# Performance work log

Measured on AMD Instinct MI355X. Metric: run time of the kernel, lower is better.

The kernel has to match this reference:

```python
import jax, jax.numpy as jnp
import numpy as np

NUM_HEADS = 16
EPS = 1e-5  # torch nn.LayerNorm default


def _ln(x, g, b):
    m = jnp.mean(x, axis=-1, keepdims=True)
    v = jnp.var(x, axis=-1, keepdims=True)
    return (x - m) / jnp.sqrt(v + EPS) * g + b


def _attn(q, k, v, proj_w, proj_b):
    B, N, C = q.shape
    S = k.shape[1]
    H = NUM_HEADS
    D = C // H
    qh = q.reshape(B, N, H, D).transpose(0, 2, 1, 3)
    kh = k.reshape(B, S, H, D).transpose(0, 2, 1, 3)
    vh = v.reshape(B, S, H, D).transpose(0, 2, 1, 3)
    scores = jnp.einsum('bhnd,bhsd->bhns', qh, kh) * (D ** -0.5)
    aw = jax.nn.softmax(scores, axis=-1)
    o = jnp.einsum('bhns,bhsd->bhnd', aw, vh)
    o = o.transpose(0, 2, 1, 3).reshape(B, N, C)
    return o @ proj_w + proj_b


def _mlp(x, w1, b1, w2, b2):
    h = jax.nn.gelu(x @ w1 + b1, approximate=False)  # torch nn.GELU (exact erf)
    return h @ w2 + b2


def setup_inputs() -> dict:
    key = jax.random.key(0)
    ks = jax.random.split(key, 12)
    B, N, C = 4, 512, 1024
    H = 4 * C
    s = 0.02
    return {
        'x': jax.random.normal(ks[0], (B, N, C), jnp.float32),
        'y': jax.random.normal(ks[1], (B, N, C), jnp.float32),
        'norm1_g': jnp.ones((C,), jnp.float32),
        'norm1_b': jnp.zeros((C,), jnp.float32),
        'norm2_g': jnp.ones((C,), jnp.float32),
        'norm2_b': jnp.zeros((C,), jnp.float32),
        'proj_w': jax.random.normal(ks[2], (C, C), jnp.float32) * s,
        'proj_b': jnp.zeros((C,), jnp.float32),
        'fc1_w': jax.random.normal(ks[3], (C, H), jnp.float32) * s,
        'fc1_b': jnp.zeros((H,), jnp.float32),
        'fc2_w': jax.random.normal(ks[4], (H, C), jnp.float32) * s,
        'fc2_b': jnp.zeros((C,), jnp.float32),
        'is_selfatt': 1,
    }


def reference(x, y, norm1_g, norm1_b, norm2_g, norm2_b, proj_w, proj_b,
              fc1_w, fc1_b, fc2_w, fc2_b, is_selfatt):
    for _ in range(4):
        if is_selfatt:
            xn = _ln(x, norm1_g, norm1_b)
            x = x + _attn(xn, xn, xn, proj_w, proj_b)
            x = x + _mlp(_ln(x, norm2_g, norm2_b), fc1_w, fc1_b, fc2_w, fc2_b)
            yn = _ln(y, norm1_g, norm1_b)
            y = y + _attn(yn, yn, yn, proj_w, proj_b)
            y = y + _mlp(_ln(y, norm2_g, norm2_b), fc1_w, fc1_b, fc2_w, fc2_b)
        xn = _ln(x, norm1_g, norm1_b)
        yn = _ln(y, norm1_g, norm1_b)
        x1 = x + _attn(xn, yn, yn, proj_w, proj_b)
        x1 = x1 + _mlp(_ln(x1, norm2_g, norm2_b), fc1_w, fc1_b, fc2_w, fc2_b)
        y1 = y + _attn(yn, xn, xn, proj_w, proj_b)
        y1 = y1 + _mlp(_ln(y1, norm2_g, norm2_b), fc1_w, fc1_b, fc2_w, fc2_b)
    return (x1, y1)
```

## Files before the change

### kernel.cpp

```cpp
#include <hip/hip_runtime.h>
#include <hip/hip_bf16.h>
#include <math.h>

#define BDIM 4
#define SEQ 512
#define CH 1024
#define NH 16
#define HD 64
#define HIDN 4096
#define ROWS (BDIM * SEQ)
#define MROWS (2 * ROWS)
#define BHTOT (BDIM * NH)

using bf16 = __hip_bfloat16;
typedef __attribute__((ext_vector_type(4))) float f32x4;
typedef __attribute__((ext_vector_type(8))) short bf16x8;

typedef __attribute__((address_space(1))) const unsigned int GU32;
typedef __attribute__((address_space(3))) unsigned int LU32;

__device__ __forceinline__ void gload16(const bf16* g, bf16* l) {
  __builtin_amdgcn_global_load_lds((GU32*)g, (LU32*)l, 16, 0, 0);
}

__global__ __launch_bounds__(256) void ln_bf16_kernel(
    const float* __restrict__ x, const float* __restrict__ g,
    const float* __restrict__ b, bf16* __restrict__ out) {
  int row = blockIdx.x;
  int t = threadIdx.x;
  const float4 v = reinterpret_cast<const float4*>(x + (size_t)row * CH)[t];
  float s = v.x + v.y + v.z + v.w;
  float s2 = v.x * v.x + v.y * v.y + v.z * v.z + v.w * v.w;
#pragma unroll
  for (int o = 32; o > 0; o >>= 1) {
    s += __shfl_down(s, o);
    s2 += __shfl_down(s2, o);
  }
  __shared__ float red[10];
  int lane = t & 63, wid = t >> 6;
  if (lane == 0) { red[wid] = s; red[4 + wid] = s2; }
  __syncthreads();
  if (t == 0) {
    float ts = red[0] + red[1] + red[2] + red[3];
    float ts2 = red[4] + red[5] + red[6] + red[7];
    float mean = ts * (1.0f / CH);
    float var = ts2 * (1.0f / CH) - mean * mean;
    red[8] = mean;
    red[9] = rsqrtf(var + 1e-5f);
  }
  __syncthreads();
  float mean = red[8], rstd = red[9];
  const float4 gv = reinterpret_cast<const float4*>(g)[t];
  const float4 bv = reinterpret_cast<const float4*>(b)[t];
  alignas(8) bf16 o4[4];
  o4[0] = __float2bfloat16((v.x - mean) * rstd * gv.x + bv.x);
  o4[1] = __float2bfloat16((v.y - mean) * rstd * gv.y + bv.y);
  o4[2] = __float2bfloat16((v.z - mean) * rstd * gv.z + bv.z);
  o4[3] = __float2bfloat16((v.w - mean) * rstd * gv.w + bv.w);
  reinterpret_cast<uint2*>(out + (size_t)row * CH)[t] = *reinterpret_cast<const uint2*>(o4);
}

__global__ __launch_bounds__(256) void head_transpose_kernel(
    const bf16* __restrict__ src, bf16* __restrict__ dst) {
  __shared__ bf16 t[32][33];
  int bh = blockIdx.z, b = bh >> 4, h = bh & 15;
  int s0 = blockIdx.x * 32, d0 = blockIdx.y * 32;
  int tx = threadIdx.x & 31, ty = threadIdx.x >> 5;
  const bf16* sp = src + ((size_t)(b * SEQ + s0)) * CH + h * HD + d0;
  for (int i = ty; i < 32; i += 8) t[i][tx] = sp[(size_t)i * CH + tx];
  __syncthreads();
  bf16* dp = dst + ((size_t)bh * HD + d0) * SEQ + s0;
  for (int i = ty; i < 32; i += 8) dp[(size_t)i * SEQ + tx] = t[tx][i];
}

__global__ __launch_bounds__(256) void wt_transpose_kernel(
    const float* __restrict__ W, bf16* __restrict__ WT, int K, int Nout) {
  __shared__ float t[32][33];
  int k0 = blockIdx.x * 32, n0 = blockIdx.y * 32;
  int tx = threadIdx.x & 31, ty = threadIdx.x >> 5;
  for (int i = ty; i < 32; i += 8)
    t[i][tx] = W[(size_t)(k0 + i) * Nout + n0 + tx];
  __syncthreads();
  for (int i = ty; i < 32; i += 8)
    WT[(size_t)(n0 + i) * K + k0 + tx] = __float2bfloat16(t[tx][i]);
}

template <int MODE, int RING>
__global__ __launch_bounds__(256) void gemm128(
    const bf16* __restrict__ A, int lda,
    const bf16* __restrict__ Bt, int ldb,
    void* __restrict__ Cout, int ldc,
    const float* __restrict__ base, const float* __restrict__ bias,
    int K) {
  int m0 = blockIdx.x * 128, n0 = blockIdx.y * 128;
  __shared__ bf16 As[RING][128 * 32];
  __shared__ bf16 Bs[RING][128 * 32];
  int tid = threadIdx.x, wid = tid >> 6, lane = tid & 63;
  int wr = wid >> 1, wc = wid & 1;
  int srow = tid >> 2;
  int scol = ((tid & 3) ^ (srow & 3)) << 3;
  const bf16* ga = &A[(size_t)(m0 + srow) * lda + scol];
  const bf16* gb = &Bt[(size_t)(n0 + srow) * ldb + scol];
  int fr = lane & 15, kr = lane >> 4;
  f32x4 acc[4][4] = {};

  auto stage = [&](int b, int k0) {
    gload16(ga + k0, As[b] + tid * 8);
    gload16(ga + (size_t)64 * lda + k0, As[b] + 2048 + tid * 8);
    gload16(gb + k0, Bs[b] + tid * 8);
    gload16(gb + (size_t)64 * ldb + k0, Bs[b] + 2048 + tid * 8);
  };
  auto compute = [&](int b) {
    bf16x8 aF[4], bF[4];
#pragma unroll
    for (int m = 0; m < 4; ++m) {
      int R = wr * 64 + m * 16 + fr;
      aF[m] = *reinterpret_cast<const bf16x8*>(&As[b][R * 32 + ((kr ^ (R & 3)) << 3)]);
    }
#pragma unroll
    for (int n = 0; n < 4; ++n) {
      int R = wc * 64 + n * 16 + fr;
      bF[n] = *reinterpret_cast<const bf16x8*>(&Bs[b][R * 32 + ((kr ^ (R & 3)) << 3)]);
    }
#pragma unroll
    for (int m = 0; m < 4; ++m)
#pragma unroll
      for (int n = 0; n < 4; ++n)
        acc[m][n] = __builtin_amdgcn_mfma_f32_16x16x32_bf16(aF[m], bF[n], acc[m][n], 0, 0, 0);
  };

  int nt = K / 32;
#pragma unroll
  for (int i = 0; i < RING - 1; ++i) stage(i, i * 32);
  for (int t = 0; t < nt; ++t) {
    int rem = nt - 1 - t;
    if (rem >= RING - 1) {
      stage((t + RING - 1) % RING, (t + RING - 1) * 32);
      if (RING == 4) asm volatile("s_waitcnt vmcnt(12)" ::: "memory");
      else           asm volatile("s_waitcnt vmcnt(8)" ::: "memory");
    } else if (rem == 2) {
      asm volatile("s_waitcnt vmcnt(8)" ::: "memory");
    } else if (rem == 1) {
      asm volatile("s_waitcnt vmcnt(4)" ::: "memory");
    } else {
      asm volatile("s_waitcnt vmcnt(0)" ::: "memory");
    }
    __builtin_amdgcn_s_barrier();
    __builtin_amdgcn_sched_barrier(0);
    compute(t % RING);
    __builtin_amdgcn_s_barrier();
  }

  int colL = lane & 15;
  int rbase = (lane >> 4) * 4;
#pragma unroll
  for (int n = 0; n < 4; ++n) {
    int gc = n0 + wc * 64 + n * 16 + colL;
    float bv = bias ? bias[gc] : 0.0f;
#pragma unroll
    for (int m = 0; m < 4; ++m)
#pragma unroll
      for (int j = 0; j < 4; ++j) {
        int gr = m0 + wr * 64 + m * 16 + rbase + j;
        float v = acc[m][n][j] + bv;
        size_t idx = (size_t)gr * ldc + gc;
        if (MODE == 0) {
          ((float*)Cout)[idx] = base[idx] + v;
        } else {
          float gl = 0.5f * v * (1.0f + erff(v * 0.70710678118654752f));
          ((bf16*)Cout)[idx] = __float2bfloat16(gl);
        }
      }
  }
}

__global__ __launch_bounds__(512) void attn_fused(
    const bf16* __restrict__ ln1, const bf16* __restrict__ vT,
    bf16* __restrict__ out, int xorb) {
  __shared__ bf16 kv[3][64 * 64];
  __shared__ bf16 Pl[128 * 512];
  int bh = blockIdx.y;
  int b = bh >> 4, h = bh & 15;
  int kvb = b ^ xorb;
  int kvbh = kvb * NH + h;
  int m0 = blockIdx.x * 128;
  int tid = threadIdx.x, wid = tid >> 6, lane = tid & 63;
  int fr = lane & 15, kr = lane >> 4;
  int srow = tid >> 3;
  int scol8 = ((tid & 7) ^ (srow & 7)) << 3;
  const bf16* kbase = ln1 + ((size_t)(kvb * SEQ + srow)) * CH + h * HD + scol8;
  const bf16* vbase = vT + ((size_t)kvbh * HD + srow) * SEQ + scol8;

  int qrow = m0 + wid * 16 + fr;
  const bf16* qbase = ln1 + ((size_t)(b * SEQ) + qrow) * CH + h * HD;
  bf16x8 qF0 = *reinterpret_cast<const bf16x8*>(qbase + kr * 8);
  bf16x8 qF1 = *reinterpret_cast<const bf16x8*>(qbase + 32 + kr * 8);

  f32x4 acc[32];
#pragma unroll
  for (int n = 0; n < 32; ++n) acc[n] = (f32x4){0.f, 0.f, 0.f, 0.f};

  gload16(kbase, kv[0] + tid * 8);
  gload16(kbase + (size_t)64 * CH, kv[1] + tid * 8);
#pragma unroll
  for (int c = 0; c < 8; ++c) {
    if (c + 2 < 8) gload16(kbase + (size_t)(c + 2) * 64 * CH, kv[(c + 2) % 3] + tid * 8);
    if (c + 2 < 8)      asm volatile("s_waitcnt vmcnt(2)" ::: "memory");
    else if (c + 1 < 8) asm volatile("s_waitcnt vmcnt(1)" ::: "memory");
    else                asm volatile("s_waitcnt vmcnt(0)" ::: "memory");
    __builtin_amdgcn_s_barrier();
    __builtin_amdgcn_sched_barrier(0);
    const char* kb = (const char*)kv[c % 3];
#pragma unroll
    for (int nf = 0; nf < 4; ++nf) {
      int sl = nf * 16 + fr;
      int byt = sl * 128 + kr * 16;
      bf16x8 k0 = *reinterpret_cast<const bf16x8*>(kb + (byt ^ ((sl & 7) << 4)));
      bf16x8 k1 = *reinterpret_cast<const bf16x8*>(kb + ((byt + 64) ^ ((sl & 7) << 4)));
      acc[c * 4 + nf] = __builtin_amdgcn_mfma_f32_16x16x32_bf16(qF0, k0, acc[c * 4 + nf], 0, 0, 0);
      acc[c * 4 + nf] = __builtin_amdgcn_mfma_f32_16x16x32_bf16(qF1, k1, acc[c * 4 + nf], 0, 0, 0);
    }
    __builtin_amdgcn_s_barrier();
  }

  float mx[4], sum[4], inv[4];
#pragma unroll
  for (int j = 0; j < 4; ++j) {
    float m = acc[0][j];
#pragma unroll
    for (int n = 1; n < 32; ++n) m = fmaxf(m, acc[n][j]);
    m = fmaxf(m, __shfl_xor(m, 1));
    m = fmaxf(m, __shfl_xor(m, 2));
    m = fmaxf(m, __shfl_xor(m, 4));
    m = fmaxf(m, __shfl_xor(m, 8));
    mx[j] = m * 0.125f;
  }
#pragma unroll
  for (int j = 0; j < 4; ++j) sum[j] = 0.f;
#pragma unroll
  for (int n = 0; n < 32; ++n)
#pragma unroll
    for (int j = 0; j < 4; ++j) {
      float p = exp2f((acc[n][j] * 0.125f - mx[j]) * 1.4426950408889634f);
      acc[n][j] = p;
      sum[j] += p;
    }
#pragma unroll
  for (int j = 0; j < 4; ++j) {
    float s = sum[j];
    s += __shfl_xor(s, 1);
    s += __shfl_xor(s, 2);
    s += __shfl_xor(s, 4);
    s += __shfl_xor(s, 8);
    inv[j] = 1.0f / s;
  }
  {
    char* pb = (char*)Pl;
#pragma unroll
    for (int n = 0; n < 32; ++n)
#pragma unroll
      for (int j = 0; j < 4; ++j) {
        int pr = wid * 16 + (lane >> 4) * 4 + j;
        int pc = fr + 16 * n;
        int byt = (pr * 1024 + pc * 2) ^ ((pr & 7) << 4);
        *reinterpret_cast<bf16*>(pb + byt) = __float2bfloat16(acc[n][j]);
      }
  }

  f32x4 oacc[4] = {};
  int prow = wid * 16 + fr;
  gload16(vbase, kv[0] + tid * 8);
  gload16(vbase + 64, kv[1] + tid * 8);
#pragma unroll
  for (int c = 0; c < 8; ++c) {
    if (c + 2 < 8) gload16(vbase + (size_t)(c + 2) * 64, kv[(c + 2) % 3] + tid * 8);
    if (c + 2 < 8)      asm volatile("s_waitcnt vmcnt(2)" ::: "memory");
    else if (c + 1 < 8) asm volatile("s_waitcnt vmcnt(1)" ::: "memory");
    else                asm volatile("s_waitcnt vmcnt(0)" ::: "memory");
    __builtin_amdgcn_s_barrier();
    __builtin_amdgcn_sched_barrier(0);
    const char* vb = (const char*)kv[c % 3];
    const char* pb = (const char*)Pl;
#pragma unroll
    for (int ks = 0; ks < 2; ++ks) {
      int pby = (prow * 1024 + (c * 64 + ks * 32 + kr * 8) * 2) ^ ((prow & 7) << 4);
      bf16x8 pF = *reinterpret_cast<const bf16x8*>(pb + pby);
#pragma unroll
      for (int nf = 0; nf < 4; ++nf) {
        int dl = nf * 16 + fr;
        int vby = (dl * 128 + ks * 64 + kr * 16) ^ ((dl & 7) << 4);
        bf16x8 vF = *reinterpret_cast<const bf16x8*>(vb + vby);
        oacc[nf] = __builtin_amdgcn_mfma_f32_16x16x32_bf16(pF, vF, oacc[nf], 0, 0, 0);
      }
    }
    __builtin_amdgcn_s_barrier();
  }

#pragma unroll
  for (int nf = 0; nf < 4; ++nf)
#pragma unroll
    for (int j = 0; j < 4; ++j) {
      int r = m0 + wid * 16 + (lane >> 4) * 4 + j;
      int d = fr + 16 * nf;
      out[((size_t)(b * SEQ) + r) * CH + h * HD + d] = __float2bfloat16(oacc[nf][j] * inv[j]);
    }
}

extern "C" void kernel_launch(void* const* d_in, const int* in_sizes, int n_in,
                              void* d_out, int out_size, void* d_ws, size_t ws_size,
                              hipStream_t stream) {
  const float* x_in  = (const float*)d_in[0];
  const float* y_in  = (const float*)d_in[1];
  const float* n1g   = (const float*)d_in[2];
  const float* n1b   = (const float*)d_in[3];
  const float* n2g   = (const float*)d_in[4];
  const float* n2b   = (const float*)d_in[5];
  const float* projw = (const float*)d_in[6];
  const float* projb = (const float*)d_in[7];
  const float* fc1w  = (const float*)d_in[8];
  const float* fc1b  = (const float*)d_in[9];
  const float* fc2w  = (const float*)d_in[10];
  const float* fc2b  = (const float*)d_in[11];

  char* p = (char*)d_ws;
  auto alloc = [&](size_t bytes) {
    char* r = p;
    p += (bytes + 255) & ~(size_t)255;
    return r;
  };
  float* xybuf  = (float*)alloc((size_t)MROWS * CH * 4);
  float* x1y1   = (float*)alloc((size_t)MROWS * CH * 4);
  bf16*  ln1out = (bf16*)alloc((size_t)MROWS * CH * 2);
  bf16*  ln2out = (bf16*)alloc((size_t)MROWS * CH * 2);
  bf16*  vTall  = (bf16*)alloc((size_t)2 * BHTOT * HD * SEQ * 2);
  bf16*  attnout= (bf16*)alloc((size_t)MROWS * CH * 2);
  bf16*  hbuf   = (bf16*)alloc((size_t)MROWS * HIDN * 2);
  bf16*  projWT = (bf16*)alloc((size_t)CH * CH * 2);
  bf16*  fc1WT  = (bf16*)alloc((size_t)HIDN * CH * 2);
  bf16*  fc2WT  = (bf16*)alloc((size_t)CH * HIDN * 2);
  if ((size_t)(p - (char*)d_ws) > ws_size) return;

  float* outxy = (float*)d_out;

  hipMemcpyAsync(xybuf, x_in, (size_t)ROWS * CH * 4, hipMemcpyDeviceToDevice, stream);
  hipMemcpyAsync(xybuf + (size_t)ROWS * CH, y_in, (size_t)ROWS * CH * 4,
                 hipMemcpyDeviceToDevice, stream);

  wt_transpose_kernel<<<dim3(CH / 32, CH / 32), 256, 0, stream>>>(projw, projWT, CH, CH);
  wt_transpose_kernel<<<dim3(CH / 32, HIDN / 32), 256, 0, stream>>>(fc1w, fc1WT, CH, HIDN);
  wt_transpose_kernel<<<dim3(HIDN / 32, CH / 32), 256, 0, stream>>>(fc2w, fc2WT, HIDN, CH);

  auto attn_all = [&](int xorb) {
    attn_fused<<<dim3(SEQ / 128, 2 * BHTOT), 512, 0, stream>>>(ln1out, vTall, attnout, xorb);
  };
  auto proj_merged = [&](const float* rbase, float* dst) {
    gemm128<0, 4><<<dim3(MROWS / 128, CH / 128), 256, 0, stream>>>(
        attnout, CH, projWT, CH, dst, CH, rbase, projb, CH);
  };
  auto mlp_merged = [&](const float* bsrc, float* dst) {
    ln_bf16_kernel<<<MROWS, 256, 0, stream>>>(bsrc, n2g, n2b, ln2out);
    gemm128<3, 3><<<dim3(MROWS / 128, HIDN / 128), 256, 0, stream>>>(
        ln2out, CH, fc1WT, CH, hbuf, HIDN, nullptr, fc1b, CH);
    gemm128<0, 4><<<dim3(MROWS / 128, CH / 128), 256, 0, stream>>>(
        hbuf, HIDN, fc2WT, HIDN, dst, CH, bsrc, fc2b, HIDN);
  };

  for (int it = 0; it < 4; ++it) {
    ln_bf16_kernel<<<MROWS, 256, 0, stream>>>(xybuf, n1g, n1b, ln1out);
    head_transpose_kernel<<<dim3(SEQ / 32, HD / 32, 2 * BHTOT), 256, 0, stream>>>(ln1out, vTall);
    attn_all(0);
    proj_merged(xybuf, xybuf);
    mlp_merged(xybuf, xybuf);
  }
  ln_bf16_kernel<<<MROWS, 256, 0, stream>>>(xybuf, n1g, n1b, ln1out);
  head_transpose_kernel<<<dim3(SEQ / 32, HD / 32, 2 * BHTOT), 256, 0, stream>>>(ln1out, vTall);
  attn_all(4);
  proj_merged(xybuf, x1y1);
  mlp_merged(x1y1, outxy);
}
```

Before: 1.194 ms.

## Use 256x256-tile GEMM for MLP and split-K fc2 with reduction kernel

Replaces the 128x128 GEMMs in the MLP with a new 256x256-tile, 512-thread GEMM that uses 64-wide K steps, double-buffered LDS and a quadrant-interleaved prefetch/MFMA schedule. fc2 is split 4 ways along K to produce enough blocks, writing fp32 partials. A separate kernel then sums the partials with the residual and bias. Larger tiles cut global and LDS traffic per FLOP. In exchange the partials add extra memory traffic and a launch, and the large tile needs more registers, which limits occupancy.

```diff
diff --git a/kernel.cpp b/kernel.cpp
--- a/kernel.cpp
+++ b/kernel.cpp
@@ -83,6 +83,25 @@
   __syncthreads();
   for (int i = ty; i < 32; i += 8)
     WT[(size_t)(n0 + i) * K + k0 + tx] = __float2bfloat16(t[tx][i]);
+}
+
+__global__ __launch_bounds__(256) void reduce4_kernel(
+    const float* __restrict__ part, const float* __restrict__ base,
+    const float* __restrict__ bias, float* __restrict__ out) {
+  size_t i = (size_t)blockIdx.x * 256 + threadIdx.x;
+  const size_t NEL = (size_t)MROWS * CH / 4;
+  float4 p0 = ((const float4*)part)[i];
+  float4 p1 = ((const float4*)part)[i + NEL];
+  float4 p2 = ((const float4*)part)[i + 2 * NEL];
+  float4 p3 = ((const float4*)part)[i + 3 * NEL];
+  float4 bs = ((const float4*)base)[i];
+  float4 bi = ((const float4*)bias)[i % (CH / 4)];
+  float4 r;
+  r.x = bs.x + p0.x + p1.x + p2.x + p3.x + bi.x;
+  r.y = bs.y + p0.y + p1.y + p2.y + p3.y + bi.y;
+  r.z = bs.z + p0.z + p1.z + p2.z + p3.z + bi.z;
+  r.w = bs.w + p0.w + p1.w + p2.w + p3.w + bi.w;
+  ((float4*)out)[i] = r;
 }
 
 template <int MODE, int RING>
@@ -174,6 +193,107 @@
   }
 }
 
+template <int MODE>
+__global__ __launch_bounds__(512, 2) void gemm256(
+    const bf16* __restrict__ A, int lda,
+    const bf16* __restrict__ Bt, int ldb,
+    void* __restrict__ Cout, int ldc,
+    const float* __restrict__ bias,
+    int Ksplit) {
+  __shared__ bf16 As[2][256 * 64];
+  __shared__ bf16 Bs[2][256 * 64];
+  int m0 = blockIdx.x * 256, n0 = blockIdx.y * 256;
+  int koff = blockIdx.z * Ksplit;
+  int tid = threadIdx.x, lane = tid & 63;
+  int wid = tid >> 6;
+  int wr = wid >> 2, wc = wid & 3;
+  int fr = lane & 15, kr = lane >> 4;
+  int sR = tid >> 3;
+  int sg = (tid & 7) ^ (sR & 7);
+  const bf16* gaBase = A + (size_t)(m0 + sR) * lda + koff + sg * 8;
+  const bf16* gbBase = Bt + (size_t)(n0 + sR) * ldb + koff + sg * 8;
+
+  f32x4 acc[8][4] = {};
+
+  auto stageA = [&](int buf, int l, int kt) {
+    gload16(gaBase + (size_t)l * 64 * lda + kt * 64, As[buf] + l * 4096 + tid * 8);
+  };
+  auto stageB = [&](int buf, int l, int kt) {
+    gload16(gbBase + (size_t)l * 64 * ldb + kt * 64, Bs[buf] + l * 4096 + tid * 8);
+  };
+  auto rdA = [&](int buf, int mf, int ks) {
+    int R = wr * 128 + mf * 16 + fr;
+    return *reinterpret_cast<const bf16x8*>(
+        &As[buf][R * 64 + (((ks * 4 + kr) ^ (R & 7)) << 3)]);
+  };
+  auto rdB = [&](int buf, int nf, int ks) {
+    int R = wc * 64 + nf * 16 + fr;
+    return *reinterpret_cast<const bf16x8*>(
+        &Bs[buf][R * 64 + (((ks * 4 + kr) ^ (R & 7)) << 3)]);
+  };
+
+  int nt = Ksplit / 64;
+#pragma unroll
+  for (int l = 0; l < 4; ++l) { stageA(0, l, 0); stageB(0, l, 0); }
+  asm volatile("s_waitcnt vmcnt(0)" ::: "memory");
+  __builtin_amdgcn_s_barrier();
+
+  bf16x8 aF[4][2], bF[4][2];
+  for (int t = 0; t < nt; ++t) {
+    int cur = t & 1, nxt = cur ^ 1;
+    bool pf = (t + 1 < nt);
+#pragma unroll
+    for (int q = 0; q < 4; ++q) {
+      if (q == 0) {
+#pragma unroll
+        for (int m = 0; m < 4; ++m) { aF[m][0] = rdA(cur, m, 0); aF[m][1] = rdA(cur, m, 1); }
+#pragma unroll
+        for (int n = 0; n < 4; ++n) { bF[n][0] = rdB(cur, n, 0); bF[n][1] = rdB(cur, n, 1); }
+      } else if (q == 2) {
+#pragma unroll
+        for (int m = 0; m < 4; ++m) { aF[m][0] = rdA(cur, 4 + m, 0); aF[m][1] = rdA(cur, 4 + m, 1); }
+      }
+      if (pf) { stageA(nxt, q, t + 1); stageB(nxt, q, t + 1); }
+      __builtin_amdgcn_s_barrier();
+      asm volatile("s_waitcnt lgkmcnt(0)" ::: "memory");
+      __builtin_amdgcn_sched_barrier(0);
+      __builtin_amdgcn_s_setprio(1);
+      int mq = (q >> 1) * 4, nq = (q & 1) * 2;
+#pragma unroll
+      for (int ks = 0; ks < 2; ++ks)
+#pragma unroll
+        for (int m = 0; m < 4; ++m)
+#pragma unroll
+          for (int n = 0; n < 2; ++n)
+            acc[mq + m][nq + n] = __builtin_amdgcn_mfma_f32_16x16x32_bf16(
+                aF[m][ks], bF[nq + n][ks], acc[mq + m][nq + n], 0, 0, 0);
+      __builtin_amdgcn_s_setprio(0);
+      if (q == 3 && pf) asm volatile("s_waitcnt vmcnt(0)" ::: "memory");
+      __builtin_amdgcn_s_barrier();
+    }
+  }
+
+  int colL = lane & 15, rb = (lane >> 4) * 4;
+#pragma unroll
+  for (int fn = 0; fn < 4; ++fn) {
+    int gc = n0 + wc * 64 + fn * 16 + colL;
+    float bv = (MODE == 3) ? bias[gc] : 0.0f;
+#pragma unroll
+    for (int fm = 0; fm < 8; ++fm)
+#pragma unroll
+      for (int j = 0; j < 4; ++j) {
+        int gr = m0 + wr * 128 + fm * 16 + rb + j;
+        float v = acc[fm][fn][j] + bv;
+        if (MODE == 3) {
+          float gl = 0.5f * v * (1.0f + erff(v * 0.70710678118654752f));
+          ((bf16*)Cout)[(size_t)gr * ldc + gc] = __float2bfloat16(gl);
+        } else {
+          ((float*)Cout)[(size_t)blockIdx.z * MROWS * ldc + (size_t)gr * ldc + gc] = v;
+        }
+      }
+  }
+}
+
 __global__ __launch_bounds__(512) void attn_fused(
     const bf16* __restrict__ ln1, const bf16* __restrict__ vT,
     bf16* __restrict__ out, int xorb) {
@@ -335,6 +455,7 @@
   bf16*  vTall  = (bf16*)alloc((size_t)2 * BHTOT * HD * SEQ * 2);
   bf16*  attnout= (bf16*)alloc((size_t)MROWS * CH * 2);
   bf16*  hbuf   = (bf16*)alloc((size_t)MROWS * HIDN * 2);
+  float* fc2part= (float*)alloc((size_t)4 * MROWS * CH * 4);
   bf16*  projWT = (bf16*)alloc((size_t)CH * CH * 2);
   bf16*  fc1WT  = (bf16*)alloc((size_t)HIDN * CH * 2);
   bf16*  fc2WT  = (bf16*)alloc((size_t)CH * HIDN * 2);
@@ -359,10 +480,11 @@
   };
   auto mlp_merged = [&](const float* bsrc, float* dst) {
     ln_bf16_kernel<<<MROWS, 256, 0, stream>>>(bsrc, n2g, n2b, ln2out);
-    gemm128<3, 3><<<dim3(MROWS / 128, HIDN / 128), 256, 0, stream>>>(
-        ln2out, CH, fc1WT, CH, hbuf, HIDN, nullptr, fc1b, CH);
-    gemm128<0, 4><<<dim3(MROWS / 128, CH / 128), 256, 0, stream>>>(
-        hbuf, HIDN, fc2WT, HIDN, dst, CH, bsrc, fc2b, HIDN);
+    gemm256<3><<<dim3(MROWS / 256, HIDN / 256, 1), 512, 0, stream>>>(
+        ln2out, CH, fc1WT, CH, hbuf, HIDN, fc1b, CH);
+    gemm256<4><<<dim3(MROWS / 256, CH / 256, 4), 512, 0, stream>>>(
+        hbuf, HIDN, fc2WT, HIDN, fc2part, CH, nullptr, HIDN / 4);
+    reduce4_kernel<<<(MROWS * CH / 4) / 256, 256, 0, stream>>>(fc2part, bsrc, fc2b, dst);
   };
 
   for (int it = 0; it < 4; ++it) {
```

Measured after the change: 1.394 ms. 1.17x slower.

## Split-K the fc2 GEMM into four partials and fuse reduction with next LayerNorm

Applied to the files above, without the earlier changes.

The fc2 GEMM (K=4096, only 16x8=128 output tiles) is split along K into four slices launched as a z-dimension, each writing fp32 partials to a new workspace buffer. A new kernel sums the partials with the residual and bias, writes the fp32 result, and computes the following norm1 LayerNorm into ln1out in the same pass. The standalone ln1 launch at the start of each iteration is removed. This targets low occupancy on a 256-CU device but adds about 32 MB of extra partial-sum traffic per MLP. The final MLP call also computes an unused LayerNorm. The variance is computed as E[x^2]-mean^2 in a single pass, which is less numerically robust.

```diff
diff --git a/kernel.cpp b/kernel.cpp
--- a/kernel.cpp
+++ b/kernel.cpp
@@ -85,6 +85,57 @@
     WT[(size_t)(n0 + i) * K + k0 + tx] = __float2bfloat16(t[tx][i]);
 }
 
+__global__ __launch_bounds__(256) void reduce4ln_kernel(
+    const float* __restrict__ part, const float* __restrict__ base,
+    const float* __restrict__ bias, const float* __restrict__ g,
+    const float* __restrict__ b, float* __restrict__ out,
+    bf16* __restrict__ lnout) {
+  int row = blockIdx.x, t = threadIdx.x;
+  size_t i = (size_t)row * 256 + t;
+  const size_t NEL = (size_t)MROWS * CH / 4;
+  float4 p0 = ((const float4*)part)[i];
+  float4 p1 = ((const float4*)part)[i + NEL];
+  float4 p2 = ((const float4*)part)[i + 2 * NEL];
+  float4 p3 = ((const float4*)part)[i + 3 * NEL];
+  float4 bs = ((const float4*)base)[i];
+  float4 bi = ((const float4*)bias)[t];
+  float4 v;
+  v.x = bs.x + p0.x + p1.x + p2.x + p3.x + bi.x;
+  v.y = bs.y + p0.y + p1.y + p2.y + p3.y + bi.y;
+  v.z = bs.z + p0.z + p1.z + p2.z + p3.z + bi.z;
+  v.w = bs.w + p0.w + p1.w + p2.w + p3.w + bi.w;
+  ((float4*)out)[i] = v;
+  float s = v.x + v.y + v.z + v.w;
+  float s2 = v.x * v.x + v.y * v.y + v.z * v.z + v.w * v.w;
+#pragma unroll
+  for (int o = 32; o > 0; o >>= 1) {
+    s += __shfl_down(s, o);
+    s2 += __shfl_down(s2, o);
+  }
+  __shared__ float red[10];
+  int lane = t & 63, wid = t >> 6;
+  if (lane == 0) { red[wid] = s; red[4 + wid] = s2; }
+  __syncthreads();
+  if (t == 0) {
+    float ts = red[0] + red[1] + red[2] + red[3];
+    float ts2 = red[4] + red[5] + red[6] + red[7];
+    float mean = ts * (1.0f / CH);
+    float var = ts2 * (1.0f / CH) - mean * mean;
+    red[8] = mean;
+    red[9] = rsqrtf(var + 1e-5f);
+  }
+  __syncthreads();
+  float mean = red[8], rstd = red[9];
+  const float4 gv = ((const float4*)g)[t];
+  const float4 bv = ((const float4*)b)[t];
+  alignas(8) bf16 o4[4];
+  o4[0] = __float2bfloat16((v.x - mean) * rstd * gv.x + bv.x);
+  o4[1] = __float2bfloat16((v.y - mean) * rstd * gv.y + bv.y);
+  o4[2] = __float2bfloat16((v.z - mean) * rstd * gv.z + bv.z);
+  o4[3] = __float2bfloat16((v.w - mean) * rstd * gv.w + bv.w);
+  reinterpret_cast<uint2*>(lnout + (size_t)row * CH)[t] = *reinterpret_cast<const uint2*>(o4);
+}
+
 template <int MODE, int RING>
 __global__ __launch_bounds__(256) void gemm128(
     const bf16* __restrict__ A, int lda,
@@ -93,14 +144,15 @@
     const float* __restrict__ base, const float* __restrict__ bias,
     int K) {
   int m0 = blockIdx.x * 128, n0 = blockIdx.y * 128;
+  int kOff = blockIdx.z * K;
   __shared__ bf16 As[RING][128 * 32];
   __shared__ bf16 Bs[RING][128 * 32];
   int tid = threadIdx.x, wid = tid >> 6, lane = tid & 63;
   int wr = wid >> 1, wc = wid & 1;
   int srow = tid >> 2;
   int scol = ((tid & 3) ^ (srow & 3)) << 3;
-  const bf16* ga = &A[(size_t)(m0 + srow) * lda + scol];
-  const bf16* gb = &Bt[(size_t)(n0 + srow) * ldb + scol];
+  const bf16* ga = &A[(size_t)(m0 + srow) * lda + kOff + scol];
+  const bf16* gb = &Bt[(size_t)(n0 + srow) * ldb + kOff + scol];
   int fr = lane & 15, kr = lane >> 4;
   f32x4 acc[4][4] = {};
 
@@ -166,9 +218,11 @@
         size_t idx = (size_t)gr * ldc + gc;
         if (MODE == 0) {
           ((float*)Cout)[idx] = base[idx] + v;
-        } else {
+        } else if (MODE == 3) {
           float gl = 0.5f * v * (1.0f + erff(v * 0.70710678118654752f));
           ((bf16*)Cout)[idx] = __float2bfloat16(gl);
+        } else {
+          ((float*)Cout)[(size_t)blockIdx.z * MROWS * ldc + idx] = v;
         }
       }
   }
@@ -335,6 +389,7 @@
   bf16*  vTall  = (bf16*)alloc((size_t)2 * BHTOT * HD * SEQ * 2);
   bf16*  attnout= (bf16*)alloc((size_t)MROWS * CH * 2);
   bf16*  hbuf   = (bf16*)alloc((size_t)MROWS * HIDN * 2);
+  float* fc2part= (float*)alloc((size_t)4 * MROWS * CH * 4);
   bf16*  projWT = (bf16*)alloc((size_t)CH * CH * 2);
   bf16*  fc1WT  = (bf16*)alloc((size_t)HIDN * CH * 2);
   bf16*  fc2WT  = (bf16*)alloc((size_t)CH * HIDN * 2);
@@ -361,18 +416,20 @@
     ln_bf16_kernel<<<MROWS, 256, 0, stream>>>(bsrc, n2g, n2b, ln2out);
     gemm128<3, 3><<<dim3(MROWS / 128, HIDN / 128), 256, 0, stream>>>(
         ln2out, CH, fc1WT, CH, hbuf, HIDN, nullptr, fc1b, CH);
-    gemm128<0, 4><<<dim3(MROWS / 128, CH / 128), 256, 0, stream>>>(
-        hbuf, HIDN, fc2WT, HIDN, dst, CH, bsrc, fc2b, HIDN);
-  };
+    gemm128<4, 4><<<dim3(MROWS / 128, CH / 128, 4), 256, 0, stream>>>(
+        hbuf, HIDN, fc2WT, HIDN, fc2part, CH, nullptr, nullptr, HIDN / 4);
+    reduce4ln_kernel<<<MROWS, 256, 0, stream>>>(
+        fc2part, bsrc, fc2b, n1g, n1b, dst, ln1out);
+  };
+
+  ln_bf16_kernel<<<MROWS, 256, 0, stream>>>(xybuf, n1g, n1b, ln1out);
 
   for (int it = 0; it < 4; ++it) {
-    ln_bf16_kernel<<<MROWS, 256, 0, stream>>>(xybuf, n1g, n1b, ln1out);
     head_transpose_kernel<<<dim3(SEQ / 32, HD / 32, 2 * BHTOT), 256, 0, stream>>>(ln1out, vTall);
     attn_all(0);
     proj_merged(xybuf, xybuf);
     mlp_merged(xybuf, xybuf);
   }
-  ln_bf16_kernel<<<MROWS, 256, 0, stream>>>(xybuf, n1g, n1b, ln1out);
   head_transpose_kernel<<<dim3(SEQ / 32, HD / 32, 2 * BHTOT), 256, 0, stream>>>(ln1out, vTall);
   attn_all(4);
   proj_merged(xybuf, x1y1);
```

After: 1.130 ms. 5.3% less time.
